# Kernel optimization log

Measured on AMD Instinct MI355X. Metric: run time of the kernel, lower is better.

Reference implementation:

```python
import jax, jax.numpy as jnp
import numpy as np

N_NODES = 100000
N_EDGES = 1600000
DIN = 128
DOUT = 128
HEADS = 4


def setup_inputs() -> dict:
    key = jax.random.key(0)
    ks = jax.random.split(key, 24)
    inp = {}
    inp['x'] = jax.random.normal(ks[0], (N_NODES, DIN), dtype=jnp.float32)
    inp['edge_index'] = jax.random.randint(ks[1], (2, N_EDGES), 0, N_NODES, dtype=jnp.int32)
    s = 0.05
    # layers 0,1: in 128 -> heads*32 = 128, concat
    for i in range(2):
        o = 4 * i
        inp[f'Wl{i}'] = jax.random.normal(ks[2 + o], (128, 128), dtype=jnp.float32) * s
        inp[f'bl{i}'] = jnp.zeros((128,), dtype=jnp.float32)
        inp[f'Wr{i}'] = jax.random.normal(ks[3 + o], (128, 128), dtype=jnp.float32) * s
        inp[f'br{i}'] = jnp.zeros((128,), dtype=jnp.float32)
        inp[f'att{i}'] = jax.random.normal(ks[4 + o], (HEADS, 32), dtype=jnp.float32) * s
        inp[f'bias{i}'] = jnp.zeros((128,), dtype=jnp.float32)
    # layer 2: in 128 -> heads*128 = 512, mean over heads -> 128
    inp['Wl2'] = jax.random.normal(ks[12], (128, 512), dtype=jnp.float32) * s
    inp['bl2'] = jnp.zeros((512,), dtype=jnp.float32)
    inp['Wr2'] = jax.random.normal(ks[13], (128, 512), dtype=jnp.float32) * s
    inp['br2'] = jnp.zeros((512,), dtype=jnp.float32)
    inp['att2'] = jax.random.normal(ks[14], (HEADS, 128), dtype=jnp.float32) * s
    inp['bias2'] = jnp.zeros((128,), dtype=jnp.float32)
    return inp


def _gatv2(h, src, dst, n, Wl, bl, Wr, br, att, bias, concat):
    H, C = att.shape
    xl = (h @ Wl + bl).reshape(n, H, C)
    xr = (h @ Wr + br).reshape(n, H, C)
    # GATv2: nonlinearity before the attention dot product
    e = jax.nn.leaky_relu(xl[src] + xr[dst], 0.2)          # [E, H, C]
    logits = jnp.einsum('ehc,hc->eh', e, att)               # [E, H]
    # segment softmax over incoming edges of each destination node
    m = jax.ops.segment_max(logits, dst, num_segments=n)    # [N, H]
    p = jnp.exp(logits - m[dst])
    denom = jax.ops.segment_sum(p, dst, num_segments=n)
    alpha = p / denom[dst]                                  # [E, H]
    out = jax.ops.segment_sum(xl[src] * alpha[:, :, None], dst, num_segments=n)  # [N, H, C]
    out = out.reshape(n, H * C) if concat else out.mean(axis=1)
    return out + bias


def reference(x, edge_index, Wl0, bl0, Wr0, br0, att0, bias0,
              Wl1, bl1, Wr1, br1, att1, bias1,
              Wl2, bl2, Wr2, br2, att2, bias2):
    n = x.shape[0]
    # add_self_loops=True (PyG GATv2Conv default)
    loops = jnp.arange(n, dtype=edge_index.dtype)
    src = jnp.concatenate([edge_index[0], loops])
    dst = jnp.concatenate([edge_index[1], loops])
    layers = [
        (Wl0, bl0, Wr0, br0, att0, bias0, True),
        (Wl1, bl1, Wr1, br1, att1, bias1, True),
        (Wl2, bl2, Wr2, br2, att2, bias2, False),
    ]
    h = x
    n_layers = len(layers)
    for i, (Wl, bl, Wr, br, att, bias, concat) in enumerate(layers):
        h = _gatv2(h, src, dst, n, Wl, bl, Wr, br, att, bias, concat)
        if i < n_layers - 1:
            h = jax.nn.elu(h)
    return h
```

## Files before the change

kernel.cpp:

```cpp
#include <hip/hip_runtime.h>
#include <hip/hip_fp16.h>
#include <cstddef>


typedef __attribute__((ext_vector_type(8))) short bf16x8;
typedef _Float16 f16x8 __attribute__((ext_vector_type(8)));
typedef __attribute__((ext_vector_type(4))) float f32x4;
typedef _Float16 f16x2 __attribute__((ext_vector_type(2)));
typedef float f32x2 __attribute__((ext_vector_type(2)));

#if defined(__has_builtin)
#if __has_builtin(__builtin_amdgcn_fdot2)
#define HAS_FDOT2 1
#endif
#endif

__device__ __forceinline__ float lrelu(float x) { return fmaxf(x, 0.2f * x); }

__device__ __forceinline__ uint4 ldrow(const void* base, unsigned byteoff) {
  return *(const uint4*)((const char*)base + byteoff);
}

__device__ __forceinline__ void split2(float x, unsigned short& h, unsigned short& l) {
  unsigned b = __float_as_uint(x);
  unsigned r = b + 0x7fffu + ((b >> 16) & 1u);
  h = (unsigned short)(r >> 16);
  float hf = __uint_as_float((unsigned)h << 16);
  float res = x - hf;
  unsigned b2 = __float_as_uint(res);
  unsigned r2 = b2 + 0x7fffu + ((b2 >> 16) & 1u);
  l = (unsigned short)(r2 >> 16);
}

__global__ void k_init(int* __restrict__ degree, int* __restrict__ cursor, int N) {
  int i = blockIdx.x * blockDim.x + threadIdx.x;
  if (i < N) { degree[i] = 1; cursor[i] = 0; }
}

__global__ void k_hist(const int* __restrict__ ei, int E, int* __restrict__ degree) {
  int e = blockIdx.x * blockDim.x + threadIdx.x;
  if (e < E) atomicAdd(&degree[ei[E + e]], 1);
}

__global__ __launch_bounds__(256) void k_scan1(const int* __restrict__ degree,
                                               int* __restrict__ partial, int N) {
  __shared__ int ws[4];
  const int i0 = blockIdx.x * 1024 + threadIdx.x * 4;
  int s = 0;
  if (i0 + 3 < N) {
    int4 v = *(const int4*)&degree[i0];
    s = v.x + v.y + v.z + v.w;
  } else {
    #pragma unroll
    for (int k = 0; k < 4; k++) if (i0 + k < N) s += degree[i0 + k];
  }
  #pragma unroll
  for (int d = 1; d < 64; d <<= 1) s += __shfl_xor(s, d);
  const int lane = threadIdx.x & 63, wid = threadIdx.x >> 6;
  if (lane == 0) ws[wid] = s;
  __syncthreads();
  if (threadIdx.x == 0) partial[blockIdx.x] = ws[0] + ws[1] + ws[2] + ws[3];
}

__global__ __launch_bounds__(256) void k_scan2(int* __restrict__ partial, int nb) {
  __shared__ int sh[256];
  const int tid = threadIdx.x;
  int v = (tid < nb) ? partial[tid] : 0;
  sh[tid] = v;
  __syncthreads();
  for (int d = 1; d < 256; d <<= 1) {
    int t = (tid >= d) ? sh[tid - d] : 0;
    __syncthreads();
    sh[tid] += t;
    __syncthreads();
  }
  if (tid < nb) partial[tid] = sh[tid] - v;
}

__global__ __launch_bounds__(256) void k_scan3(const int* __restrict__ degree,
                                               const int* __restrict__ partial,
                                               int* __restrict__ offs, int N) {
  __shared__ int wsum[4];
  const int tid = threadIdx.x, lane = tid & 63, wid = tid >> 6;
  const int i0 = blockIdx.x * 1024 + tid * 4;
  int v0 = 0, v1 = 0, v2 = 0, v3 = 0;
  if (i0 + 3 < N) {
    int4 v = *(const int4*)&degree[i0];
    v0 = v.x; v1 = v.y; v2 = v.z; v3 = v.w;
  } else {
    if (i0     < N) v0 = degree[i0];
    if (i0 + 1 < N) v1 = degree[i0 + 1];
    if (i0 + 2 < N) v2 = degree[i0 + 2];
    if (i0 + 3 < N) v3 = degree[i0 + 3];
  }
  int s = v0 + v1 + v2 + v3, x = s;
  #pragma unroll
  for (int d = 1; d < 64; d <<= 1) {
    int y = __shfl_up(x, d);
    if (lane >= d) x += y;
  }
  if (lane == 63) wsum[wid] = x;
  __syncthreads();
  if (tid < 4) {
    int t = wsum[tid];
    #pragma unroll
    for (int d = 1; d < 4; d <<= 1) {
      int y = __shfl_up(t, d);
      if (tid >= d) t += y;
    }
    wsum[tid] = t;
  }
  __syncthreads();
  const int wbase = wid ? wsum[wid - 1] : 0;
  int e = partial[blockIdx.x] + wbase + (x - s);
  if (i0     < N) offs[i0]     = e;  e += v0;  if (i0     == N - 1) offs[N] = e;
  if (i0 + 1 < N) offs[i0 + 1] = e;  e += v1;  if (i0 + 1 == N - 1) offs[N] = e;
  if (i0 + 2 < N) offs[i0 + 2] = e;  e += v2;  if (i0 + 2 == N - 1) offs[N] = e;
  if (i0 + 3 < N) offs[i0 + 3] = e;  e += v3;  if (i0 + 3 == N - 1) offs[N] = e;
}

__global__ void k_scatter(const int* __restrict__ ei, int E, int N,
                          const int* __restrict__ offs, int* __restrict__ cursor,
                          int* __restrict__ csr_src) {
  int t = blockIdx.x * blockDim.x + threadIdx.x;
  int ET = E + N;
  if (t >= ET) return;
  int s, d;
  if (t < E) { s = ei[t]; d = ei[E + t]; }
  else       { s = t - E; d = s; }
  int pos = offs[d] + atomicAdd(&cursor[d], 1);
  csr_src[pos] = s;
}

__global__ __launch_bounds__(256) void k_prep(
    const float* __restrict__ Wl0, const float* __restrict__ Wr0,
    const float* __restrict__ Wl1, const float* __restrict__ Wr1,
    const float* __restrict__ Wl2, const float* __restrict__ Wr2,
    unsigned short* __restrict__ W0hl, unsigned short* __restrict__ W0ll,
    unsigned short* __restrict__ W0hr, unsigned short* __restrict__ W0lr,
    unsigned short* __restrict__ W1hl, unsigned short* __restrict__ W1ll,
    unsigned short* __restrict__ W1hr, unsigned short* __restrict__ W1lr,
    unsigned short* __restrict__ W2hl, unsigned short* __restrict__ W2ll,
    unsigned short* __restrict__ W2hr, unsigned short* __restrict__ W2lr,
    __half* __restrict__ W0fl, __half* __restrict__ W0fr,
    __half* __restrict__ W1fl, __half* __restrict__ W1fr,
    __half* __restrict__ W2fl, __half* __restrict__ W2fr,
    const float* __restrict__ X, __half* __restrict__ A16x,
    unsigned short* __restrict__ Ah, unsigned short* __restrict__ Al,
    int totalA, int fusedF) {
  const int t = blockIdx.x * blockDim.x + threadIdx.x;
  if (t < 196608) {
    const float* W; unsigned short *Whp, *Wlp; int idx, sh;
    if (t < 16384)       { W = Wl0; Whp = W0hl; Wlp = W0ll; idx = t;          sh = 7; }
    else if (t < 32768)  { W = Wr0; Whp = W0hr; Wlp = W0lr; idx = t - 16384;  sh = 7; }
    else if (t < 49152)  { W = Wl1; Whp = W1hl; Wlp = W1ll; idx = t - 32768;  sh = 7; }
    else if (t < 65536)  { W = Wr1; Whp = W1hr; Wlp = W1lr; idx = t - 49152;  sh = 7; }
    else if (t < 131072) { W = Wl2; Whp = W2hl; Wlp = W2ll; idx = t - 65536;  sh = 9; }
    else                 { W = Wr2; Whp = W2hr; Wlp = W2lr; idx = t - 131072; sh = 9; }
    const int n = idx & ((1 << sh) - 1), k = idx >> sh;
    unsigned short h, l;
    split2(W[idx], h, l);
    Whp[(size_t)n * 128 + k] = h;
    Wlp[(size_t)n * 128 + k] = l;
    return;
  }
  if (t < 327680) {
    const int u = t - 196608;
    const float* W = (u < 65536) ? Wl2 : Wr2;
    __half* O = (u < 65536) ? W2fl : W2fr;
    const int idx = (u < 65536) ? u : u - 65536;
    const int n = idx & 511, k = idx >> 9;
    O[(size_t)n * 128 + k] = __float2half(W[idx]);
    return;
  }
  if (t < 393216) {
    const int u = t - 327680;
    const float* W; __half* O; int idx;
    if (u < 16384)      { W = Wl0; O = W0fl; idx = u; }
    else if (u < 32768) { W = Wr0; O = W0fr; idx = u - 16384; }
    else if (u < 49152) { W = Wl1; O = W1fl; idx = u - 32768; }
    else                { W = Wr1; O = W1fr; idx = u - 49152; }
    const int n = idx & 127, k = idx >> 7;
    O[(size_t)n * 128 + k] = __float2half(W[idx]);
    return;
  }
  const int t4 = (t - 393216) * 4;
  if (t4 >= totalA) return;
  float4 v = *(const float4*)&X[t4];
  if (fusedF) {
    union { uint2 u; __half h[4]; } ou;
    ou.h[0] = __float2half(v.x); ou.h[1] = __float2half(v.y);
    ou.h[2] = __float2half(v.z); ou.h[3] = __float2half(v.w);
    *(uint2*)&A16x[t4] = ou.u;
  } else {
    unsigned short h0, h1, h2, h3, l0, l1, l2, l3;
    split2(v.x, h0, l0); split2(v.y, h1, l1);
    split2(v.z, h2, l2); split2(v.w, h3, l3);
    uint2 hv, lv;
    hv.x = (unsigned)h0 | ((unsigned)h1 << 16);
    hv.y = (unsigned)h2 | ((unsigned)h3 << 16);
    lv.x = (unsigned)l0 | ((unsigned)l1 << 16);
    lv.y = (unsigned)l2 | ((unsigned)l3 << 16);
    *(uint2*)&Ah[t4] = hv;
    *(uint2*)&Al[t4] = lv;
  }
}

__global__ __launch_bounds__(256) void k_gemm2s(
    const unsigned short* __restrict__ Agh, const unsigned short* __restrict__ Agl,
    const unsigned short* __restrict__ Whl, const unsigned short* __restrict__ Wll,
    const unsigned short* __restrict__ Whr, const unsigned short* __restrict__ Wlr,
    const float* __restrict__ bias_l, const float* __restrict__ bias_r,
    void* __restrict__ Clp, void* __restrict__ Crp, int N,
    int ldC, int coloff, int out_half) {
  __shared__ unsigned short Ah_s[128][40];
  __shared__ unsigned short Al_s[128][40];
  __shared__ unsigned short Wh_s[128][40];
  __shared__ unsigned short Wl_s[128][40];
  const int hsel = blockIdx.z;
  const unsigned short* __restrict__ Wth = (blockIdx.y ? Whr : Whl) + hsel * 128 * 128;
  const unsigned short* __restrict__ Wtl = (blockIdx.y ? Wlr : Wll) + hsel * 128 * 128;
  const float* __restrict__ bias = (blockIdx.y ? bias_r : bias_l) + hsel * 128;
  void* __restrict__ Cp = blockIdx.y ? Crp : Clp;
  coloff += hsel * 128;

  const int tid = threadIdx.x;
  const int m0 = blockIdx.x * 128;
  const int wv = tid >> 6, lane = tid & 63;
  const int wm = (wv >> 1) * 64, wn = (wv & 1) * 64;
  const int l15 = lane & 15, kb = (lane >> 4) * 8;
  f32x4 acc[4][4] = {};

  const int r = tid >> 1;
  const int cb = (tid & 1) * 16;
  const bool arow_ok = (m0 + r) < N;
  const unsigned short* ahp = Agh + (size_t)(m0 + r) * 128 + cb;
  const unsigned short* alp = Agl + (size_t)(m0 + r) * 128 + cb;
  const unsigned short* whp = Wth + r * 128 + cb;
  const unsigned short* wlp = Wtl + r * 128 + cb;
  const uint4 z4 = make_uint4(0, 0, 0, 0);

  uint4 pa0, pa1, pl0, pl1, pw0, pw1, pq0, pq1;
  #define LOADC(K0)                                                           \
    pa0 = arow_ok ? *(const uint4*)(ahp + (K0))     : z4;                     \
    pa1 = arow_ok ? *(const uint4*)(ahp + (K0) + 8) : z4;                     \
    pl0 = arow_ok ? *(const uint4*)(alp + (K0))     : z4;                     \
    pl1 = arow_ok ? *(const uint4*)(alp + (K0) + 8) : z4;                     \
    pw0 = *(const uint4*)(whp + (K0));                                        \
    pw1 = *(const uint4*)(whp + (K0) + 8);                                    \
    pq0 = *(const uint4*)(wlp + (K0));                                        \
    pq1 = *(const uint4*)(wlp + (K0) + 8);
  LOADC(0)
  for (int kc = 0; kc < 4; kc++) {
    *(uint4*)&Ah_s[r][cb]     = pa0;
    *(uint4*)&Ah_s[r][cb + 8] = pa1;
    *(uint4*)&Al_s[r][cb]     = pl0;
    *(uint4*)&Al_s[r][cb + 8] = pl1;
    *(uint4*)&Wh_s[r][cb]     = pw0;
    *(uint4*)&Wh_s[r][cb + 8] = pw1;
    *(uint4*)&Wl_s[r][cb]     = pq0;
    *(uint4*)&Wl_s[r][cb + 8] = pq1;
    __syncthreads();
    if (kc < 3) { LOADC((kc + 1) * 32) }

    bf16x8 afh[4], afl[4];
    #pragma unroll
    for (int mi = 0; mi < 4; mi++) {
      const int row = wm + mi * 16 + l15;
      afh[mi] = *(const bf16x8*)&Ah_s[row][kb];
      afl[mi] = *(const bf16x8*)&Al_s[row][kb];
    }
    #pragma unroll
    for (int ni = 0; ni < 4; ni++) {
      const int rown = wn + ni * 16 + l15;
      bf16x8 bh = *(const bf16x8*)&Wh_s[rown][kb];
      bf16x8 bl = *(const bf16x8*)&Wl_s[rown][kb];
      #pragma unroll
      for (int mi = 0; mi < 4; mi++) {
        acc[mi][ni] = __builtin_amdgcn_mfma_f32_16x16x32_bf16(afh[mi], bh, acc[mi][ni], 0, 0, 0);
        acc[mi][ni] = __builtin_amdgcn_mfma_f32_16x16x32_bf16(afl[mi], bh, acc[mi][ni], 0, 0, 0);
        acc[mi][ni] = __builtin_amdgcn_mfma_f32_16x16x32_bf16(afh[mi], bl, acc[mi][ni], 0, 0, 0);
      }
    }
    __syncthreads();
  }
  #undef LOADC
  const int col = l15, rbase = (lane >> 4) * 4;
  #pragma unroll
  for (int ni = 0; ni < 4; ni++) {
    const int gn = wn + ni * 16 + col;
    const float bv = bias[gn];
    #pragma unroll
    for (int mi = 0; mi < 4; mi++) {
      #pragma unroll
      for (int q = 0; q < 4; q++) {
        const int gm = m0 + wm + mi * 16 + rbase + q;
        if (gm < N) {
          float v = acc[mi][ni][q] + bv;
          if (out_half) ((__half*)Cp)[(size_t)gm * ldC + coloff + gn] = __float2half(v);
          else          ((float*)Cp)[(size_t)gm * ldC + coloff + gn] = v;
        }
      }
    }
  }
}

__global__ __launch_bounds__(256) void k_gemm2h(
    const __half* __restrict__ A16,
    const __half* __restrict__ Wfl, const __half* __restrict__ Wfr,
    const float* __restrict__ bias_l, const float* __restrict__ bias_r,
    __half* __restrict__ Clp, __half* __restrict__ Crp, int N, int ldC) {
  __shared__ __half A_s[128][40];
  __shared__ __half W_s[128][40];
  const int hsel = blockIdx.z;
  const __half* __restrict__ Wt = (blockIdx.y ? Wfr : Wfl) + hsel * 128 * 128;
  const float* __restrict__ bias = (blockIdx.y ? bias_r : bias_l) + hsel * 128;
  __half* __restrict__ Cp = blockIdx.y ? Crp : Clp;
  const int coloff = hsel * 128;

  const int tid = threadIdx.x;
  const int m0 = blockIdx.x * 128;
  const int wv = tid >> 6, lane = tid & 63;
  const int wm = (wv >> 1) * 64, wn = (wv & 1) * 64;
  const int l15 = lane & 15, kb = (lane >> 4) * 8;
  f32x4 acc[4][4] = {};

  const int r = tid >> 1;
  const int cb = (tid & 1) * 16;
  const bool arow_ok = (m0 + r) < N;
  const __half* ap = A16 + (size_t)(m0 + r) * 128 + cb;
  const __half* wp = Wt + r * 128 + cb;
  const uint4 z4 = make_uint4(0, 0, 0, 0);

  uint4 pa0, pa1, pw0, pw1;
  #define LOADH(K0)                                                           \
    pa0 = arow_ok ? *(const uint4*)(ap + (K0))     : z4;                      \
    pa1 = arow_ok ? *(const uint4*)(ap + (K0) + 8) : z4;                      \
    pw0 = *(const uint4*)(wp + (K0));                                         \
    pw1 = *(const uint4*)(wp + (K0) + 8);
  LOADH(0)
  for (int kc = 0; kc < 4; kc++) {
    *(uint4*)&A_s[r][cb]     = pa0;
    *(uint4*)&A_s[r][cb + 8] = pa1;
    *(uint4*)&W_s[r][cb]     = pw0;
    *(uint4*)&W_s[r][cb + 8] = pw1;
    __syncthreads();
    if (kc < 3) { LOADH((kc + 1) * 32) }

    f16x8 af[4];
    #pragma unroll
    for (int mi = 0; mi < 4; mi++)
      af[mi] = *(const f16x8*)&A_s[wm + mi * 16 + l15][kb];
    #pragma unroll
    for (int ni = 0; ni < 4; ni++) {
      f16x8 bh = *(const f16x8*)&W_s[wn + ni * 16 + l15][kb];
      #pragma unroll
      for (int mi = 0; mi < 4; mi++)
        acc[mi][ni] = __builtin_amdgcn_mfma_f32_16x16x32_f16(af[mi], bh, acc[mi][ni], 0, 0, 0);
    }
    __syncthreads();
  }
  #undef LOADH
  const int col = l15, rbase = (lane >> 4) * 4;
  #pragma unroll
  for (int ni = 0; ni < 4; ni++) {
    const int gn = wn + ni * 16 + col;
    const float bv = bias[gn];
    #pragma unroll
    for (int mi = 0; mi < 4; mi++) {
      #pragma unroll
      for (int q = 0; q < 4; q++) {
        const int gm = m0 + wm + mi * 16 + rbase + q;
        if (gm < N)
          Cp[(size_t)gm * ldC + coloff + gn] = __float2half(acc[mi][ni][q] + bv);
      }
    }
  }
}

#define MERGE_ADD(d)                                                          \
  {                                                                           \
    l += __shfl_xor(l, d);                                                    \
    aca.x += __shfl_xor(aca.x, d); aca.y += __shfl_xor(aca.y, d);             \
    aca.z += __shfl_xor(aca.z, d); aca.w += __shfl_xor(aca.w, d);             \
    acb.x += __shfl_xor(acb.x, d); acb.y += __shfl_xor(acb.y, d);             \
    acb.z += __shfl_xor(acb.z, d); acb.w += __shfl_xor(acb.w, d);             \
  }

__global__ __launch_bounds__(256) void k_gat_small(
    const float* __restrict__ xl, const float* __restrict__ xr,
    const float* __restrict__ att, const float* __restrict__ bias,
    const int* __restrict__ offs, const int* __restrict__ degree,
    const int* __restrict__ csr_src,
    unsigned short* __restrict__ Ah, unsigned short* __restrict__ Al, int N) {
  const int node = blockIdx.x * 4 + (threadIdx.x >> 6);
  if (node >= N) return;
  const int lane = threadIdx.x & 63;
  const int g = lane >> 4;
  const int c = lane & 15;
  const int d0 = c * 8;
  const size_t nb = (size_t)node * 128 + d0;
  const float4 xra = *(const float4*)&xr[nb];
  const float4 xrb = *(const float4*)&xr[nb + 4];
  const float4 ata = *(const float4*)&att[d0];
  const float4 atb = *(const float4*)&att[d0 + 4];
  const int off = offs[node];
  const int deg = degree[node];
  float l = 0.f;
  float4 aca = make_float4(0.f, 0.f, 0.f, 0.f);
  float4 acb = make_float4(0.f, 0.f, 0.f, 0.f);
  int s0 = (g < deg) ? csr_src[off + g] : 0;
  int s1 = (g + 4 < deg) ? csr_src[off + g + 4] : 0;
  for (int j = g; j < deg; j += 8) {
    int sn0 = (j + 8 < deg) ? csr_src[off + j + 8] : 0;
    int sn1 = (j + 12 < deg) ? csr_src[off + j + 12] : 0;
    const size_t sb0 = (size_t)s0 * 128 + d0;
    const size_t sb1 = (size_t)s1 * 128 + d0;
    float4 xa0 = *(const float4*)&xl[sb0];
    float4 xb0 = *(const float4*)&xl[sb0 + 4];
    float4 xa1 = *(const float4*)&xl[sb1];
    float4 xb1 = *(const float4*)&xl[sb1 + 4];
    float t0 = lrelu(xa0.x + xra.x) * ata.x + lrelu(xa0.y + xra.y) * ata.y +
               lrelu(xa0.z + xra.z) * ata.z + lrelu(xa0.w + xra.w) * ata.w +
               lrelu(xb0.x + xrb.x) * atb.x + lrelu(xb0.y + xrb.y) * atb.y +
               lrelu(xb0.z + xrb.z) * atb.z + lrelu(xb0.w + xrb.w) * atb.w;
    float t1 = lrelu(xa1.x + xra.x) * ata.x + lrelu(xa1.y + xra.y) * ata.y +
               lrelu(xa1.z + xra.z) * ata.z + lrelu(xa1.w + xra.w) * ata.w +
               lrelu(xb1.x + xrb.x) * atb.x + lrelu(xb1.y + xrb.y) * atb.y +
               lrelu(xb1.z + xrb.z) * atb.z + lrelu(xb1.w + xrb.w) * atb.w;
    t0 += __shfl_xor(t0, 1);
    t0 += __shfl_xor(t0, 2);
    t1 += __shfl_xor(t1, 1);
    t1 += __shfl_xor(t1, 2);
    float p0 = __expf(t0);
    float p1 = (j + 4 < deg) ? __expf(t1) : 0.f;
    aca.x += p0 * xa0.x + p1 * xa1.x; aca.y += p0 * xa0.y + p1 * xa1.y;
    aca.z += p0 * xa0.z + p1 * xa1.z; aca.w += p0 * xa0.w + p1 * xa1.w;
    acb.x += p0 * xb0.x + p1 * xb1.x; acb.y += p0 * xb0.y + p1 * xb1.y;
    acb.z += p0 * xb0.z + p1 * xb1.z; acb.w += p0 * xb0.w + p1 * xb1.w;
    l += p0 + p1;
    s0 = sn0; s1 = sn1;
  }
  MERGE_ADD(16)
  MERGE_ADD(32)
  if (lane < 16) {
    const float inv = 1.f / l;
    const float4 b0 = *(const float4*)&bias[d0];
    const float4 b1 = *(const float4*)&bias[d0 + 4];
    float o[8] = {aca.x * inv + b0.x, aca.y * inv + b0.y,
                  aca.z * inv + b0.z, aca.w * inv + b0.w,
                  acb.x * inv + b1.x, acb.y * inv + b1.y,
                  acb.z * inv + b1.z, acb.w * inv + b1.w};
    unsigned short hs[8], ls[8];
    #pragma unroll
    for (int i = 0; i < 8; i++) {
      o[i] = o[i] > 0.f ? o[i] : __expf(o[i]) - 1.f;
      split2(o[i], hs[i], ls[i]);
    }
    uint4 hv, lv;
    hv.x = (unsigned)hs[0] | ((unsigned)hs[1] << 16);
    hv.y = (unsigned)hs[2] | ((unsigned)hs[3] << 16);
    hv.z = (unsigned)hs[4] | ((unsigned)hs[5] << 16);
    hv.w = (unsigned)hs[6] | ((unsigned)hs[7] << 16);
    lv.x = (unsigned)ls[0] | ((unsigned)ls[1] << 16);
    lv.y = (unsigned)ls[2] | ((unsigned)ls[3] << 16);
    lv.z = (unsigned)ls[4] | ((unsigned)ls[5] << 16);
    lv.w = (unsigned)ls[6] | ((unsigned)ls[7] << 16);
    *(uint4*)&Ah[nb] = hv;
    *(uint4*)&Al[nb] = lv;
  }
}

__device__ __forceinline__ void edge_step(uint4 vv, bool valid,
                                          const f16x2* xrh, const f16x2* ath,
                                          f32x2* accv, float& l) {
  union { uint4 u; f16x2 h[4]; } xu; xu.u = vv;
  const f16x2 c02 = {(_Float16)0.2f, (_Float16)0.2f};
  float t = 0.f;
#if defined(HAS_FDOT2)
  #pragma unroll
  for (int i = 0; i < 4; i++) {
    f16x2 s = xu.h[i] + xrh[i];
    f16x2 lr = __builtin_elementwise_max(s, s * c02);
    t = __builtin_amdgcn_fdot2(lr, ath[i], t, false);
  }
#else
  #pragma unroll
  for (int i = 0; i < 4; i++) {
    f32x2 s = __builtin_convertvector(xu.h[i], f32x2) +
              __builtin_convertvector(xrh[i], f32x2);
    f32x2 a = __builtin_convertvector(ath[i], f32x2);
    t += fmaxf(s.x, 0.2f * s.x) * a.x + fmaxf(s.y, 0.2f * s.y) * a.y;
  }
#endif
  t += __shfl_xor(t, 1);
  t += __shfl_xor(t, 2);
  t += __shfl_xor(t, 4);
  t += __shfl_xor(t, 8);
  float p = valid ? __expf(t) : 0.f;
  l += p;
  f32x2 p2 = {p, p};
  #pragma unroll
  for (int i = 0; i < 4; i++)
    accv[i] += p2 * __builtin_convertvector(xu.h[i], f32x2);
}

__device__ __forceinline__ void edge_step_small(uint4 vv,
                                                const f16x2* xrh, const f16x2* ath,
                                                f32x2* accv, float& l) {
  union { uint4 u; f16x2 h[4]; } xu; xu.u = vv;
  const f16x2 c02 = {(_Float16)0.2f, (_Float16)0.2f};
  float t = 0.f;
#if defined(HAS_FDOT2)
  #pragma unroll
  for (int i = 0; i < 4; i++) {
    f16x2 s = xu.h[i] + xrh[i];
    f16x2 lr = __builtin_elementwise_max(s, s * c02);
    t = __builtin_amdgcn_fdot2(lr, ath[i], t, false);
  }
#else
  #pragma unroll
  for (int i = 0; i < 4; i++) {
    f32x2 s = __builtin_convertvector(xu.h[i], f32x2) +
              __builtin_convertvector(xrh[i], f32x2);
    f32x2 a = __builtin_convertvector(ath[i], f32x2);
    t += fmaxf(s.x, 0.2f * s.x) * a.x + fmaxf(s.y, 0.2f * s.y) * a.y;
  }
#endif
  t += __shfl_xor(t, 1);
  t += __shfl_xor(t, 2);
  float p = __expf(t);
  l += p;
  f32x2 p2 = {p, p};
  #pragma unroll
  for (int i = 0; i < 4; i++)
    accv[i] += p2 * __builtin_convertvector(xu.h[i], f32x2);
}

__global__ __launch_bounds__(256) void k_gat_small16(
    const __half* __restrict__ xl, const __half* __restrict__ xr,
    const float* __restrict__ att, const float* __restrict__ bias,
    const int* __restrict__ offs, const int* __restrict__ degree,
    const int* __restrict__ csr_src,
    unsigned short* __restrict__ Ah, unsigned short* __restrict__ Al,
    __half* __restrict__ A16, int mode, int N) {
  const int node = blockIdx.x * 4 + (threadIdx.x >> 6);
  if (node >= N) return;
  const int lane = threadIdx.x & 63;
  const int g = lane >> 4;
  const int c = lane & 15;
  const int d0 = c * 8;
  f16x2 xrh[4], ath[4];
  {
    union { uint4 u; f16x2 h[4]; } ru;
    ru.u = *(const uint4*)&xr[(size_t)node * 128 + d0];
    float4 a0 = *(const float4*)&att[d0];
    float4 a1 = *(const float4*)&att[d0 + 4];
    #pragma unroll
    for (int i = 0; i < 4; i++) xrh[i] = ru.h[i];
    ath[0] = (f16x2){(_Float16)a0.x, (_Float16)a0.y};
    ath[1] = (f16x2){(_Float16)a0.z, (_Float16)a0.w};
    ath[2] = (f16x2){(_Float16)a1.x, (_Float16)a1.y};
    ath[3] = (f16x2){(_Float16)a1.z, (_Float16)a1.w};
  }
  const int off = offs[node];
  const int deg = degree[node];
  const unsigned lb = (unsigned)d0 * 2u;
  f32x2 accv[4] = {};
  float l = 0.f;
  int ia = (g < deg)     ? csr_src[off + g]     : 0;
  int ib = (g + 4 < deg) ? csr_src[off + g + 4] : 0;
  int ic = (g + 8 < deg) ? csr_src[off + g + 8] : 0;
  uint4 v0 = make_uint4(0, 0, 0, 0), v1 = v0;
  if (g < deg)     v0 = ldrow(xl, (unsigned)ia * 256u + lb);
  if (g + 4 < deg) v1 = ldrow(xl, (unsigned)ib * 256u + lb);
  for (int j = g; j < deg; j += 4) {
    uint4 vn = v0;
    if (j + 8 < deg) vn = ldrow(xl, (unsigned)ic * 256u + lb);
    int id = (j + 12 < deg) ? csr_src[off + j + 12] : 0;
    edge_step_small(v0, xrh, ath, accv, l);
    v0 = v1; v1 = vn; ic = id;
  }
  #pragma unroll
  for (int d = 16; d < 64; d <<= 1) {
    l += __shfl_xor(l, d);
    #pragma unroll
    for (int i = 0; i < 4; i++) {
      accv[i].x += __shfl_xor(accv[i].x, d);
      accv[i].y += __shfl_xor(accv[i].y, d);
    }
  }
  if (lane < 16) {
    const float inv = 1.f / l;
    const float4 b0 = *(const float4*)&bias[d0];
    const float4 b1 = *(const float4*)&bias[d0 + 4];
    float o[8] = {accv[0].x * inv + b0.x, accv[0].y * inv + b0.y,
                  accv[1].x * inv + b0.z, accv[1].y * inv + b0.w,
                  accv[2].x * inv + b1.x, accv[2].y * inv + b1.y,
                  accv[3].x * inv + b1.z, accv[3].y * inv + b1.w};
    #pragma unroll
    for (int i = 0; i < 8; i++)
      o[i] = o[i] > 0.f ? o[i] : __expf(o[i]) - 1.f;
    const size_t nb = (size_t)node * 128 + d0;
    if (mode == 1) {
      union { uint4 u; __half h[8]; } ou;
      #pragma unroll
      for (int i = 0; i < 8; i++) ou.h[i] = __float2half(o[i]);
      *(uint4*)&A16[nb] = ou.u;
    } else {
      unsigned short hs[8], ls[8];
      #pragma unroll
      for (int i = 0; i < 8; i++) split2(o[i], hs[i], ls[i]);
      uint4 hv, lv;
      hv.x = (unsigned)hs[0] | ((unsigned)hs[1] << 16);
      hv.y = (unsigned)hs[2] | ((unsigned)hs[3] << 16);
      hv.z = (unsigned)hs[4] | ((unsigned)hs[5] << 16);
      hv.w = (unsigned)hs[6] | ((unsigned)hs[7] << 16);
      lv.x = (unsigned)ls[0] | ((unsigned)ls[1] << 16);
      lv.y = (unsigned)ls[2] | ((unsigned)ls[3] << 16);
      lv.z = (unsigned)ls[4] | ((unsigned)ls[5] << 16);
      lv.w = (unsigned)ls[6] | ((unsigned)ls[7] << 16);
      *(uint4*)&Ah[nb] = hv;
      *(uint4*)&Al[nb] = lv;
    }
  }
}

__global__ __launch_bounds__(256) void k_gat_fused4(
    const __half* __restrict__ xl4, const __half* __restrict__ xr4,
    const float* __restrict__ att2, const float* __restrict__ bias,
    const int* __restrict__ offs, const int* __restrict__ degree,
    const int* __restrict__ csr_src, float* __restrict__ out, int N) {
  const int node = blockIdx.x * 4 + (threadIdx.x >> 6);
  if (node >= N) return;
  const int lane = threadIdx.x & 63;
  f16x2 xrh[4], ath[4];
  {
    union { uint4 u; f16x2 h[4]; } ru;
    ru.u = *(const uint4*)&xr4[(size_t)node * 512 + lane * 8];
    float4 a0 = *(const float4*)&att2[lane * 8];
    float4 a1 = *(const float4*)&att2[lane * 8 + 4];
    #pragma unroll
    for (int i = 0; i < 4; i++) xrh[i] = ru.h[i];
    ath[0] = (f16x2){(_Float16)a0.x, (_Float16)a0.y};
    ath[1] = (f16x2){(_Float16)a0.z, (_Float16)a0.w};
    ath[2] = (f16x2){(_Float16)a1.x, (_Float16)a1.y};
    ath[3] = (f16x2){(_Float16)a1.z, (_Float16)a1.w};
  }
  const int off = offs[node];
  const int deg = degree[node];
  const unsigned lb = (unsigned)lane * 16u;
  f32x2 accv[4] = {};
  float l = 0.f;
  int s0 = csr_src[off];
  int s1 = (1 < deg) ? csr_src[off + 1] : 0;
  int s2 = (2 < deg) ? csr_src[off + 2] : 0;
  int s3 = (3 < deg) ? csr_src[off + 3] : 0;
  uint4 v0 = ldrow(xl4, (unsigned)s0 * 1024u + lb);
  uint4 v1 = (1 < deg) ? ldrow(xl4, (unsigned)s1 * 1024u + lb) : v0;
  uint4 v2 = (2 < deg) ? ldrow(xl4, (unsigned)s2 * 1024u + lb) : v0;
  uint4 v3 = (3 < deg) ? ldrow(xl4, (unsigned)s3 * 1024u + lb) : v0;
  s0 = (4 < deg) ? csr_src[off + 4] : 0;
  s1 = (5 < deg) ? csr_src[off + 5] : 0;
  s2 = (6 < deg) ? csr_src[off + 6] : 0;
  s3 = (7 < deg) ? csr_src[off + 7] : 0;
  for (int j = 0; j < deg; j += 4) {
    edge_step(v0, true, xrh, ath, accv, l);
    if (j + 4 < deg) v0 = ldrow(xl4, (unsigned)s0 * 1024u + lb);
    s0 = (j + 8 < deg) ? csr_src[off + j + 8] : 0;
    edge_step(v1, j + 1 < deg, xrh, ath, accv, l);
    if (j + 5 < deg) v1 = ldrow(xl4, (unsigned)s1 * 1024u + lb);
    s1 = (j + 9 < deg) ? csr_src[off + j + 9] : 0;
    edge_step(v2, j + 2 < deg, xrh, ath, accv, l);
    if (j + 6 < deg) v2 = ldrow(xl4, (unsigned)s2 * 1024u + lb);
    s2 = (j + 10 < deg) ? csr_src[off + j + 10] : 0;
    edge_step(v3, j + 3 < deg, xrh, ath, accv, l);
    if (j + 7 < deg) v3 = ldrow(xl4, (unsigned)s3 * 1024u + lb);
    s3 = (j + 11 < deg) ? csr_src[off + j + 11] : 0;
  }
  const float w = 0.25f / l;
  const f32x2 w2 = {w, w};
  #pragma unroll
  for (int i = 0; i < 4; i++) accv[i] *= w2;
  #pragma unroll
  for (int d = 16; d < 64; d <<= 1) {
    #pragma unroll
    for (int i = 0; i < 4; i++) {
      accv[i].x += __shfl_xor(accv[i].x, d);
      accv[i].y += __shfl_xor(accv[i].y, d);
    }
  }
  if (lane < 16) {
    const int d0 = lane * 8;
    float4 b0 = *(const float4*)&bias[d0];
    float4 b1 = *(const float4*)&bias[d0 + 4];
    float* op = &out[(size_t)node * 128 + d0];
    *(float4*)op       = make_float4(accv[0].x + b0.x, accv[0].y + b0.y,
                                     accv[1].x + b0.z, accv[1].y + b0.w);
    *(float4*)(op + 4) = make_float4(accv[2].x + b1.x, accv[2].y + b1.y,
                                     accv[3].x + b1.z, accv[3].y + b1.w);
  }
}

__global__ __launch_bounds__(256) void k_gat_head(
    const float* __restrict__ xl, const float* __restrict__ xr,
    const float* __restrict__ att_h, const float* __restrict__ bias,
    const int* __restrict__ offs, const int* __restrict__ degree,
    const int* __restrict__ csr_src, float* __restrict__ out, int N,
    int first, int last) {
  const int node = blockIdx.x * 4 + (threadIdx.x >> 6);
  if (node >= N) return;
  const int lane = threadIdx.x & 63;
  const int g = lane >> 4;
  const int c = lane & 15;
  const int d0 = c * 8;
  const size_t nb = (size_t)node * 128 + d0;
  const float4 xra = *(const float4*)&xr[nb];
  const float4 xrb = *(const float4*)&xr[nb + 4];
  const float4 ata = *(const float4*)&att_h[d0];
  const float4 atb = *(const float4*)&att_h[d0 + 4];
  const int off = offs[node];
  const int deg = degree[node];
  float l = 0.f;
  float4 aca = make_float4(0.f, 0.f, 0.f, 0.f);
  float4 acb = make_float4(0.f, 0.f, 0.f, 0.f);
  int s0 = (g < deg) ? csr_src[off + g] : 0;
  int s1 = (g + 4 < deg) ? csr_src[off + g + 4] : 0;
  for (int j = g; j < deg; j += 8) {
    int sn0 = (j + 8 < deg) ? csr_src[off + j + 8] : 0;
    int sn1 = (j + 12 < deg) ? csr_src[off + j + 12] : 0;
    const size_t sb0 = (size_t)s0 * 128 + d0;
    const size_t sb1 = (size_t)s1 * 128 + d0;
    float4 xa0 = *(const float4*)&xl[sb0];
    float4 xb0 = *(const float4*)&xl[sb0 + 4];
    float4 xa1 = *(const float4*)&xl[sb1];
    float4 xb1 = *(const float4*)&xl[sb1 + 4];
    float t0 = lrelu(xa0.x + xra.x) * ata.x + lrelu(xa0.y + xra.y) * ata.y +
               lrelu(xa0.z + xra.z) * ata.z + lrelu(xa0.w + xra.w) * ata.w +
               lrelu(xb0.x + xrb.x) * atb.x + lrelu(xb0.y + xrb.y) * atb.y +
               lrelu(xb0.z + xrb.z) * atb.z + lrelu(xb0.w + xrb.w) * atb.w;
    float t1 = lrelu(xa1.x + xra.x) * ata.x + lrelu(xa1.y + xra.y) * ata.y +
               lrelu(xa1.z + xra.z) * ata.z + lrelu(xa1.w + xra.w) * ata.w +
               lrelu(xb1.x + xrb.x) * atb.x + lrelu(xb1.y + xrb.y) * atb.y +
               lrelu(xb1.z + xrb.z) * atb.z + lrelu(xb1.w + xrb.w) * atb.w;
    t0 += __shfl_xor(t0, 1);
    t0 += __shfl_xor(t0, 2);
    t0 += __shfl_xor(t0, 4);
    t0 += __shfl_xor(t0, 8);
    t1 += __shfl_xor(t1, 1);
    t1 += __shfl_xor(t1, 2);
    t1 += __shfl_xor(t1, 4);
    t1 += __shfl_xor(t1, 8);
    float p0 = __expf(t0);
    float p1 = (j + 4 < deg) ? __expf(t1) : 0.f;
    aca.x += p0 * xa0.x + p1 * xa1.x; aca.y += p0 * xa0.y + p1 * xa1.y;
    aca.z += p0 * xa0.z + p1 * xa1.z; aca.w += p0 * xa0.w + p1 * xa1.w;
    acb.x += p0 * xb0.x + p1 * xb1.x; acb.y += p0 * xb0.y + p1 * xb1.y;
    acb.z += p0 * xb0.z + p1 * xb1.z; acb.w += p0 * xb0.w + p1 * xb1.w;
    l += p0 + p1;
    s0 = sn0; s1 = sn1;
  }
  MERGE_ADD(16)
  MERGE_ADD(32)
  if (lane < 16) {
    const float inv = 0.25f / l;
    float o[8] = {aca.x * inv, aca.y * inv, aca.z * inv, aca.w * inv,
                  acb.x * inv, acb.y * inv, acb.z * inv, acb.w * inv};
    float* op = &out[nb];
    if (!first) {
      float4 p0 = *(const float4*)op;
      float4 p1 = *(const float4*)(op + 4);
      o[0] += p0.x; o[1] += p0.y; o[2] += p0.z; o[3] += p0.w;
      o[4] += p1.x; o[5] += p1.y; o[6] += p1.z; o[7] += p1.w;
    }
    if (last) {
      float4 b0 = *(const float4*)&bias[d0];
      float4 b1 = *(const float4*)&bias[d0 + 4];
      o[0] += b0.x; o[1] += b0.y; o[2] += b0.z; o[3] += b0.w;
      o[4] += b1.x; o[5] += b1.y; o[6] += b1.z; o[7] += b1.w;
    }
    *(float4*)op       = make_float4(o[0], o[1], o[2], o[3]);
    *(float4*)(op + 4) = make_float4(o[4], o[5], o[6], o[7]);
  }
}

extern "C" void kernel_launch(void* const* d_in, const int* in_sizes, int n_in,
                              void* d_out, int out_size, void* d_ws, size_t ws_size,
                              hipStream_t stream) {
  const float* x     = (const float*)d_in[0];
  const int*   ei    = (const int*)  d_in[1];
  const float* Wl0   = (const float*)d_in[2];
  const float* bl0   = (const float*)d_in[3];
  const float* Wr0   = (const float*)d_in[4];
  const float* br0   = (const float*)d_in[5];
  const float* att0  = (const float*)d_in[6];
  const float* bias0 = (const float*)d_in[7];
  const float* Wl1   = (const float*)d_in[8];
  const float* bl1   = (const float*)d_in[9];
  const float* Wr1   = (const float*)d_in[10];
  const float* br1   = (const float*)d_in[11];
  const float* att1  = (const float*)d_in[12];
  const float* bias1 = (const float*)d_in[13];
  const float* Wl2   = (const float*)d_in[14];
  const float* bl2   = (const float*)d_in[15];
  const float* Wr2   = (const float*)d_in[16];
  const float* br2   = (const float*)d_in[17];
  const float* att2  = (const float*)d_in[18];
  const float* bias2 = (const float*)d_in[19];

  const int N = in_sizes[0] / 128;
  const int E = in_sizes[1] / 2;

  char* p = (char*)d_ws;
  auto alloc = [&](size_t bytes) {
    void* q = (void*)p;
    p += (bytes + 255) & ~(size_t)255;
    return q;
  };
  auto al = [](size_t b) { return (b + 255) & ~(size_t)255; };
  const size_t common = al((size_t)(N + 1) * 4) + 2 * al((size_t)N * 4) +
                        al((size_t)(E + N) * 4) + al((size_t)512) +
                        2 * al((size_t)N * 128 * 2) +
                        8 * al((size_t)128 * 128 * 2) +
                        4 * al((size_t)512 * 128 * 2) +
                        2 * al((size_t)512 * 128 * 2) +
                        4 * al((size_t)128 * 128 * 2);
  const size_t need_fused = common + 2 * al((size_t)N * 512 * 2);
  const bool fused = ws_size >= need_fused;

  int* offs    = (int*)alloc((size_t)(N + 1) * 4);
  int* degree  = (int*)alloc((size_t)N * 4);
  int* cursor  = (int*)alloc((size_t)N * 4);
  int* csr_src = (int*)alloc((size_t)(E + N) * 4);
  int* partial = (int*)alloc((size_t)512);
  unsigned short* Agh = (unsigned short*)alloc((size_t)N * 128 * 2);
  unsigned short* Agl = (unsigned short*)alloc((size_t)N * 128 * 2);
  unsigned short* W0hl = (unsigned short*)alloc((size_t)128 * 128 * 2);
  unsigned short* W0ll = (unsigned short*)alloc((size_t)128 * 128 * 2);
  unsigned short* W0hr = (unsigned short*)alloc((size_t)128 * 128 * 2);
  unsigned short* W0lr = (unsigned short*)alloc((size_t)128 * 128 * 2);
  unsigned short* W1hl = (unsigned short*)alloc((size_t)128 * 128 * 2);
  unsigned short* W1ll = (unsigned short*)alloc((size_t)128 * 128 * 2);
  unsigned short* W1hr = (unsigned short*)alloc((size_t)128 * 128 * 2);
  unsigned short* W1lr = (unsigned short*)alloc((size_t)128 * 128 * 2);
  unsigned short* W2hl = (unsigned short*)alloc((size_t)512 * 128 * 2);
  unsigned short* W2ll = (unsigned short*)alloc((size_t)512 * 128 * 2);
  unsigned short* W2hr = (unsigned short*)alloc((size_t)512 * 128 * 2);
  unsigned short* W2lr = (unsigned short*)alloc((size_t)512 * 128 * 2);
  __half* W2fl = (__half*)alloc((size_t)512 * 128 * 2);
  __half* W2fr = (__half*)alloc((size_t)512 * 128 * 2);
  __half* W0fl = (__half*)alloc((size_t)128 * 128 * 2);
  __half* W0fr = (__half*)alloc((size_t)128 * 128 * 2);
  __half* W1fl = (__half*)alloc((size_t)128 * 128 * 2);
  __half* W1fr = (__half*)alloc((size_t)128 * 128 * 2);
  __half* xl4 = nullptr; __half* xr4 = nullptr;
  float* xl = nullptr; float* xr = nullptr;
  __half* xl16 = nullptr; __half* xr16 = nullptr;
  if (fused) {
    xl4 = (__half*)alloc((size_t)N * 512 * 2);
    xr4 = (__half*)alloc((size_t)N * 512 * 2);
    xl16 = xl4;
    xr16 = xr4;
  } else {
    xl = (float*)alloc((size_t)N * 128 * 4);
    xr = (float*)alloc((size_t)N * 128 * 4);
  }
  __half* A16x = (__half*)Agl;
  __half* A16a = (__half*)Agh;
  __half* A16b = (__half*)Agl;
  (void)n_in; (void)out_size;

  const int nb = (N + 1023) / 1024;

  k_init<<<(N + 255) / 256, 256, 0, stream>>>(degree, cursor, N);
  k_hist<<<(E + 255) / 256, 256, 0, stream>>>(ei, E, degree);
  k_scan1<<<nb, 256, 0, stream>>>(degree, partial, N);
  k_scan2<<<1, 256, 0, stream>>>(partial, nb);
  k_scan3<<<nb, 256, 0, stream>>>(degree, partial, offs, N);
  k_scatter<<<(E + N + 255) / 256, 256, 0, stream>>>(ei, E, N, offs, cursor, csr_src);

  const int prepT = 393216 + (N * 128 + 3) / 4;
  k_prep<<<(prepT + 255) / 256, 256, 0, stream>>>(
      Wl0, Wr0, Wl1, Wr1, Wl2, Wr2,
      W0hl, W0ll, W0hr, W0lr, W1hl, W1ll, W1hr, W1lr,
      W2hl, W2ll, W2hr, W2lr,
      W0fl, W0fr, W1fl, W1fr, W2fl, W2fr,
      x, A16x, Agh, Agl, N * 128, fused ? 1 : 0);

  const int mb = (N + 127) / 128;
  const dim3 gg(mb, 2);
  const dim3 gg4(mb, 2, 4);
  const int gb = (N + 3) / 4;

  if (fused) {
    k_gemm2h<<<gg, 256, 0, stream>>>(A16x, W0fl, W0fr, bl0, br0,
                                     xl16, xr16, N, 128);
    k_gat_small16<<<gb, 256, 0, stream>>>(xl16, xr16, att0, bias0, offs, degree,
                                          csr_src, nullptr, nullptr, A16a, 1, N);
    k_gemm2h<<<gg, 256, 0, stream>>>(A16a, W1fl, W1fr, bl1, br1,
                                     xl16, xr16, N, 128);
    k_gat_small16<<<gb, 256, 0, stream>>>(xl16, xr16, att1, bias1, offs, degree,
                                          csr_src, nullptr, nullptr, A16b, 1, N);
    k_gemm2h<<<gg4, 256, 0, stream>>>(A16b, W2fl, W2fr, bl2, br2,
                                      xl4, xr4, N, 512);
    k_gat_fused4<<<gb, 256, 0, stream>>>(xl4, xr4, att2, bias2, offs, degree,
                                         csr_src, (float*)d_out, N);
  } else {
    k_gemm2s<<<gg, 256, 0, stream>>>(Agh, Agl, W0hl, W0ll, W0hr, W0lr,
                                     bl0, br0, xl, xr, N, 128, 0, 0);
    k_gat_small<<<gb, 256, 0, stream>>>(xl, xr, att0, bias0, offs, degree, csr_src,
                                        Agh, Agl, N);
    k_gemm2s<<<gg, 256, 0, stream>>>(Agh, Agl, W1hl, W1ll, W1hr, W1lr,
                                     bl1, br1, xl, xr, N, 128, 0, 0);
    k_gat_small<<<gb, 256, 0, stream>>>(xl, xr, att1, bias1, offs, degree, csr_src,
                                        Agh, Agl, N);
    for (int h = 0; h < 4; h++) {
      const int wo = h * 128 * 128;
      k_gemm2s<<<gg, 256, 0, stream>>>(Agh, Agl, W2hl + wo, W2ll + wo,
                                       W2hr + wo, W2lr + wo,
                                       bl2 + h * 128, br2 + h * 128,
                                       xl, xr, N, 128, 0, 0);
      k_gat_head<<<gb, 256, 0, stream>>>(xl, xr, att2 + h * 128, bias2, offs, degree,
                                         csr_src, (float*)d_out, N,
                                         h == 0 ? 1 : 0, h == 3 ? 1 : 0);
    }
  }
}
```

Measured before the change: 924.2 us.

## Accumulate GAT edge aggregation in fp16, stage GEMM stores, fuse init into prep

Edge aggregation in both GAT kernels now accumulates the weighted neighbour rows in packed fp16 instead of fp32. This halves the multiply-add work per edge but risks precision loss and overflow, since unnormalised exp weights summed over high-degree nodes can exceed fp16 range. The fp16 GEMM epilogue now stages outputs through shared memory and writes coalesced 16-byte rows instead of scattered half stores. The degree/cursor init kernel is folded into the prep kernel, which also skips converting weights it does not need in the selected path.

```diff
diff --git a/kernel.cpp b/kernel.cpp
--- a/kernel.cpp
+++ b/kernel.cpp
@@ -30,11 +30,6 @@
   unsigned b2 = __float_as_uint(res);
   unsigned r2 = b2 + 0x7fffu + ((b2 >> 16) & 1u);
   l = (unsigned short)(r2 >> 16);
-}
-
-__global__ void k_init(int* __restrict__ degree, int* __restrict__ cursor, int N) {
-  int i = blockIdx.x * blockDim.x + threadIdx.x;
-  if (i < N) { degree[i] = 1; cursor[i] = 0; }
 }
 
 __global__ void k_hist(const int* __restrict__ ei, int E, int* __restrict__ degree) {
@@ -147,63 +142,61 @@
     __half* __restrict__ W2fl, __half* __restrict__ W2fr,
     const float* __restrict__ X, __half* __restrict__ A16x,
     unsigned short* __restrict__ Ah, unsigned short* __restrict__ Al,
-    int totalA, int fusedF) {
+    int totalA, int N, int fusedF,
+    int* __restrict__ degree, int* __restrict__ cursor) {
   const int t = blockIdx.x * blockDim.x + threadIdx.x;
+  const int NA4 = totalA >> 2;
   if (t < 196608) {
-    const float* W; unsigned short *Whp, *Wlp; int idx, sh;
-    if (t < 16384)       { W = Wl0; Whp = W0hl; Wlp = W0ll; idx = t;          sh = 7; }
-    else if (t < 32768)  { W = Wr0; Whp = W0hr; Wlp = W0lr; idx = t - 16384;  sh = 7; }
-    else if (t < 49152)  { W = Wl1; Whp = W1hl; Wlp = W1ll; idx = t - 32768;  sh = 7; }
-    else if (t < 65536)  { W = Wr1; Whp = W1hr; Wlp = W1lr; idx = t - 49152;  sh = 7; }
-    else if (t < 131072) { W = Wl2; Whp = W2hl; Wlp = W2ll; idx = t - 65536;  sh = 9; }
-    else                 { W = Wr2; Whp = W2hr; Wlp = W2lr; idx = t - 131072; sh = 9; }
-    const int n = idx & ((1 << sh) - 1), k = idx >> sh;
-    unsigned short h, l;
-    split2(W[idx], h, l);
-    Whp[(size_t)n * 128 + k] = h;
-    Wlp[(size_t)n * 128 + k] = l;
+    if (fusedF) {
+      const float* W; __half* O; int idx, sh;
+      if (t < 16384)       { W = Wl0; O = W0fl; idx = t;          sh = 7; }
+      else if (t < 32768)  { W = Wr0; O = W0fr; idx = t - 16384;  sh = 7; }
+      else if (t < 49152)  { W = Wl1; O = W1fl; idx = t - 32768;  sh = 7; }
+      else if (t < 65536)  { W = Wr1; O = W1fr; idx = t - 49152;  sh = 7; }
+      else if (t < 131072) { W = Wl2; O = W2fl; idx = t - 65536;  sh = 9; }
+      else                 { W = Wr2; O = W2fr; idx = t - 131072; sh = 9; }
+      const int n = idx & ((1 << sh) - 1), k = idx >> sh;
+      O[(size_t)n * 128 + k] = __float2half(W[idx]);
+    } else {
+      const float* W; unsigned short *Whp, *Wlp; int idx, sh;
+      if (t < 16384)       { W = Wl0; Whp = W0hl; Wlp = W0ll; idx = t;          sh = 7; }
+      else if (t < 32768)  { W = Wr0; Whp = W0hr; Wlp = W0lr; idx = t - 16384;  sh = 7; }
+      else if (t < 49152)  { W = Wl1; Whp = W1hl; Wlp = W1ll; idx = t - 32768;  sh = 7; }
+      else if (t < 65536)  { W = Wr1; Whp = W1hr; Wlp = W1lr; idx = t - 49152;  sh = 7; }
+      else if (t < 131072) { W = Wl2; Whp = W2hl; Wlp = W2ll; idx = t - 65536;  sh = 9; }
+      else                 { W = Wr2; Whp = W2hr; Wlp = W2lr; idx = t - 131072; sh = 9; }
+      const int n = idx & ((1 << sh) - 1), k = idx >> sh;
+      unsigned short h, l;
+      split2(W[idx], h, l);
+      Whp[(size_t)n * 128 + k] = h;
+      Wlp[(size_t)n * 128 + k] = l;
+    }
     return;
   }
-  if (t < 327680) {
-    const int u = t - 196608;
-    const float* W = (u < 65536) ? Wl2 : Wr2;
-    __half* O = (u < 65536) ? W2fl : W2fr;
-    const int idx = (u < 65536) ? u : u - 65536;
-    const int n = idx & 511, k = idx >> 9;
-    O[(size_t)n * 128 + k] = __float2half(W[idx]);
+  if (t < 196608 + NA4) {
+    const int t4 = (t - 196608) * 4;
+    float4 v = *(const float4*)&X[t4];
+    if (fusedF) {
+      union { uint2 u; __half h[4]; } ou;
+      ou.h[0] = __float2half(v.x); ou.h[1] = __float2half(v.y);
+      ou.h[2] = __float2half(v.z); ou.h[3] = __float2half(v.w);
+      *(uint2*)&A16x[t4] = ou.u;
+    } else {
+      unsigned short h0, h1, h2, h3, l0, l1, l2, l3;
+      split2(v.x, h0, l0); split2(v.y, h1, l1);
+      split2(v.z, h2, l2); split2(v.w, h3, l3);
+      uint2 hv, lv;
+      hv.x = (unsigned)h0 | ((unsigned)h1 << 16);
+      hv.y = (unsigned)h2 | ((unsigned)h3 << 16);
+      lv.x = (unsigned)l0 | ((unsigned)l1 << 16);
+      lv.y = (unsigned)l2 | ((unsigned)l3 << 16);
+      *(uint2*)&Ah[t4] = hv;
+      *(uint2*)&Al[t4] = lv;
+    }
     return;
   }
-  if (t < 393216) {
-    const int u = t - 327680;
-    const float* W; __half* O; int idx;
-    if (u < 16384)      { W = Wl0; O = W0fl; idx = u; }
-    else if (u < 32768) { W = Wr0; O = W0fr; idx = u - 16384; }
-    else if (u < 49152) { W = Wl1; O = W1fl; idx = u - 32768; }
-    else                { W = Wr1; O = W1fr; idx = u - 49152; }
-    const int n = idx & 127, k = idx >> 7;
-    O[(size_t)n * 128 + k] = __float2half(W[idx]);
-    return;
-  }
-  const int t4 = (t - 393216) * 4;
-  if (t4 >= totalA) return;
-  float4 v = *(const float4*)&X[t4];
-  if (fusedF) {
-    union { uint2 u; __half h[4]; } ou;
-    ou.h[0] = __float2half(v.x); ou.h[1] = __float2half(v.y);
-    ou.h[2] = __float2half(v.z); ou.h[3] = __float2half(v.w);
-    *(uint2*)&A16x[t4] = ou.u;
-  } else {
-    unsigned short h0, h1, h2, h3, l0, l1, l2, l3;
-    split2(v.x, h0, l0); split2(v.y, h1, l1);
-    split2(v.z, h2, l2); split2(v.w, h3, l3);
-    uint2 hv, lv;
-    hv.x = (unsigned)h0 | ((unsigned)h1 << 16);
-    hv.y = (unsigned)h2 | ((unsigned)h3 << 16);
-    lv.x = (unsigned)l0 | ((unsigned)l1 << 16);
-    lv.y = (unsigned)l2 | ((unsigned)l3 << 16);
-    *(uint2*)&Ah[t4] = hv;
-    *(uint2*)&Al[t4] = lv;
-  }
+  const int i = t - 196608 - NA4;
+  if (i < N) { degree[i] = 1; cursor[i] = 0; }
 }
 
 __global__ __launch_bounds__(256) void k_gemm2s(
@@ -310,8 +303,9 @@
     const __half* __restrict__ Wfl, const __half* __restrict__ Wfr,
     const float* __restrict__ bias_l, const float* __restrict__ bias_r,
     __half* __restrict__ Clp, __half* __restrict__ Crp, int N, int ldC) {
-  __shared__ __half A_s[128][40];
-  __shared__ __half W_s[128][40];
+  __shared__ __align__(16) unsigned char smem[20480];
+  __half (* __restrict__ A_s)[40] = (__half(*)[40])smem;
+  __half (* __restrict__ W_s)[40] = (__half(*)[40])(smem + 10240);
   const int hsel = blockIdx.z;
   const __half* __restrict__ Wt = (blockIdx.y ? Wfr : Wfl) + hsel * 128 * 128;
   const float* __restrict__ bias = (blockIdx.y ? bias_r : bias_l) + hsel * 128;
@@ -361,20 +355,34 @@
     __syncthreads();
   }
   #undef LOADH
+  __half* C_s = (__half*)smem;
   const int col = l15, rbase = (lane >> 4) * 4;
   #pragma unroll
-  for (int ni = 0; ni < 4; ni++) {
-    const int gn = wn + ni * 16 + col;
-    const float bv = bias[gn];
-    #pragma unroll
-    for (int mi = 0; mi < 4; mi++) {
+  for (int hp = 0; hp < 2; hp++) {
+    if ((wv >> 1) == hp) {
       #pragma unroll
-      for (int q = 0; q < 4; q++) {
-        const int gm = m0 + wm + mi * 16 + rbase + q;
-        if (gm < N)
-          Cp[(size_t)gm * ldC + coloff + gn] = __float2half(acc[mi][ni][q] + bv);
+      for (int ni = 0; ni < 4; ni++) {
+        const int gn = wn + ni * 16 + col;
+        const float bv = bias[gn];
+        #pragma unroll
+        for (int mi = 0; mi < 4; mi++) {
+          #pragma unroll
+          for (int q = 0; q < 4; q++)
+            C_s[(mi * 16 + rbase + q) * 136 + gn] = __float2half(acc[mi][ni][q] + bv);
+        }
       }
     }
+    __syncthreads();
+    #pragma unroll
+    for (int i = 0; i < 4; i++) {
+      const int flat = tid + i * 256;
+      const int row = flat >> 4, c16 = flat & 15;
+      const int gm = m0 + hp * 64 + row;
+      if (gm < N)
+        *(uint4*)(Cp + (size_t)gm * ldC + coloff + c16 * 8) =
+            *(const uint4*)(C_s + row * 136 + c16 * 8);
+    }
+    __syncthreads();
   }
 }
 
@@ -473,7 +481,7 @@
 
 __device__ __forceinline__ void edge_step(uint4 vv, bool valid,
                                           const f16x2* xrh, const f16x2* ath,
-                                          f32x2* accv, float& l) {
+                                          f16x2* acc16, float& l) {
   union { uint4 u; f16x2 h[4]; } xu; xu.u = vv;
   const f16x2 c02 = {(_Float16)0.2f, (_Float16)0.2f};
   float t = 0.f;
@@ -499,15 +507,16 @@
   t += __shfl_xor(t, 8);
   float p = valid ? __expf(t) : 0.f;
   l += p;
-  f32x2 p2 = {p, p};
+  const _Float16 ph = (_Float16)p;
+  const f16x2 p2 = {ph, ph};
   #pragma unroll
   for (int i = 0; i < 4; i++)
-    accv[i] += p2 * __builtin_convertvector(xu.h[i], f32x2);
+    acc16[i] += p2 * xu.h[i];
 }
 
 __device__ __forceinline__ void edge_step_small(uint4 vv,
                                                 const f16x2* xrh, const f16x2* ath,
-                                                f32x2* accv, float& l) {
+                                                f16x2* acc16, float& l) {
   union { uint4 u; f16x2 h[4]; } xu; xu.u = vv;
   const f16x2 c02 = {(_Float16)0.2f, (_Float16)0.2f};
   float t = 0.f;
@@ -531,10 +540,11 @@
   t += __shfl_xor(t, 2);
   float p = __expf(t);
   l += p;
-  f32x2 p2 = {p, p};
+  const _Float16 ph = (_Float16)p;
+  const f16x2 p2 = {ph, ph};
   #pragma unroll
   for (int i = 0; i < 4; i++)
-    accv[i] += p2 * __builtin_convertvector(xu.h[i], f32x2);
+    acc16[i] += p2 * xu.h[i];
 }
 
 __global__ __launch_bounds__(256) void k_gat_small16(
@@ -566,7 +576,7 @@
   const int off = offs[node];
   const int deg = degree[node];
   const unsigned lb = (unsigned)d0 * 2u;
-  f32x2 accv[4] = {};
+  f16x2 acc16[4] = {};
   float l = 0.f;
   int ia = (g < deg)     ? csr_src[off + g]     : 0;
   int ib = (g + 4 < deg) ? csr_src[off + g + 4] : 0;
@@ -578,9 +588,12 @@
     uint4 vn = v0;
     if (j + 8 < deg) vn = ldrow(xl, (unsigned)ic * 256u + lb);
     int id = (j + 12 < deg) ? csr_src[off + j + 12] : 0;
-    edge_step_small(v0, xrh, ath, accv, l);
+    edge_step_small(v0, xrh, ath, acc16, l);
     v0 = v1; v1 = vn; ic = id;
   }
+  f32x2 accv[4];
+  #pragma unroll
+  for (int i = 0; i < 4; i++) accv[i] = __builtin_convertvector(acc16[i], f32x2);
   #pragma unroll
   for (int d = 16; d < 64; d <<= 1) {
     l += __shfl_xor(l, d);
@@ -650,7 +663,7 @@
   const int off = offs[node];
   const int deg = degree[node];
   const unsigned lb = (unsigned)lane * 16u;
-  f32x2 accv[4] = {};
+  f16x2 acc16[4] = {};
   float l = 0.f;
   int s0 = csr_src[off];
   int s1 = (1 < deg) ? csr_src[off + 1] : 0;
@@ -665,19 +678,22 @@
   s2 = (6 < deg) ? csr_src[off + 6] : 0;
   s3 = (7 < deg) ? csr_src[off + 7] : 0;
   for (int j = 0; j < deg; j += 4) {
-    edge_step(v0, true, xrh, ath, accv, l);
+    edge_step(v0, true, xrh, ath, acc16, l);
     if (j + 4 < deg) v0 = ldrow(xl4, (unsigned)s0 * 1024u + lb);
     s0 = (j + 8 < deg) ? csr_src[off + j + 8] : 0;
-    edge_step(v1, j + 1 < deg, xrh, ath, accv, l);
+    edge_step(v1, j + 1 < deg, xrh, ath, acc16, l);
     if (j + 5 < deg) v1 = ldrow(xl4, (unsigned)s1 * 1024u + lb);
     s1 = (j + 9 < deg) ? csr_src[off + j + 9] : 0;
-    edge_step(v2, j + 2 < deg, xrh, ath, accv, l);
+    edge_step(v2, j + 2 < deg, xrh, ath, acc16, l);
     if (j + 6 < deg) v2 = ldrow(xl4, (unsigned)s2 * 1024u + lb);
     s2 = (j + 10 < deg) ? csr_src[off + j + 10] : 0;
-    edge_step(v3, j + 3 < deg, xrh, ath, accv, l);
+    edge_step(v3, j + 3 < deg, xrh, ath, acc16, l);
     if (j + 7 < deg) v3 = ldrow(xl4, (unsigned)s3 * 1024u + lb);
     s3 = (j + 11 < deg) ? csr_src[off + j + 11] : 0;
   }
+  f32x2 accv[4];
+  #pragma unroll
+  for (int i = 0; i < 4; i++) accv[i] = __builtin_convertvector(acc16[i], f32x2);
   const float w = 0.25f / l;
   const f32x2 w2 = {w, w};
   #pragma unroll
@@ -872,20 +888,20 @@
 
   const int nb = (N + 1023) / 1024;
 
-  k_init<<<(N + 255) / 256, 256, 0, stream>>>(degree, cursor, N);
+  const int NA4 = (N * 128) / 4;
+  const int prepT = 196608 + NA4 + N;
+  k_prep<<<(prepT + 255) / 256, 256, 0, stream>>>(
+      Wl0, Wr0, Wl1, Wr1, Wl2, Wr2,
+      W0hl, W0ll, W0hr, W0lr, W1hl, W1ll, W1hr, W1lr,
+      W2hl, W2ll, W2hr, W2lr,
+      W0fl, W0fr, W1fl, W1fr, W2fl, W2fr,
+      x, A16x, Agh, Agl, N * 128, N, fused ? 1 : 0, degree, cursor);
+
   k_hist<<<(E + 255) / 256, 256, 0, stream>>>(ei, E, degree);
   k_scan1<<<nb, 256, 0, stream>>>(degree, partial, N);
   k_scan2<<<1, 256, 0, stream>>>(partial, nb);
   k_scan3<<<nb, 256, 0, stream>>>(degree, partial, offs, N);
   k_scatter<<<(E + N + 255) / 256, 256, 0, stream>>>(ei, E, N, offs, cursor, csr_src);
-
-  const int prepT = 393216 + (N * 128 + 3) / 4;
-  k_prep<<<(prepT + 255) / 256, 256, 0, stream>>>(
-      Wl0, Wr0, Wl1, Wr1, Wl2, Wr2,
-      W0hl, W0ll, W0hr, W0lr, W1hl, W1ll, W1hr, W1lr,
-      W2hl, W2ll, W2hr, W2lr,
-      W0fl, W0fr, W1fl, W1fr, W2fl, W2fr,
-      x, A16x, Agh, Agl, N * 128, fused ? 1 : 0);
 
   const int mb = (N + 127) / 128;
   const dim3 gg(mb, 2);
```

New measurement: 808.9 us. -12.5%, faster.
